# Performance work log

Hardware: AMD Instinct MI355X
Metric: run time of the kernel (lower is better)

The kernel has to match this reference:

```python
import jax, jax.numpy as jnp
import numpy as np

EPS = 1e-5  # torch BatchNorm1d default eps


def _bn(x, gamma, beta):
    # training-mode batch norm over axis 0 (biased variance, like torch)
    m = x.mean(axis=0)
    v = x.var(axis=0)
    return (x - m) * jax.lax.rsqrt(v + EPS) * gamma + beta


def setup_inputs() -> dict:
    key = jax.random.key(0)
    ks = jax.random.split(key, 6)
    B, T, D_IN, E, H, D_OUT = 8192, 64, 2, 128, 128, 5
    s = 0.05
    f32 = jnp.float32
    return {
        "inputs": jax.random.normal(ks[0], (B, T, D_IN), f32),
        # input BatchNorm1d(2)
        "in_gamma": jnp.ones((D_IN,), f32),
        "in_beta": jnp.zeros((D_IN,), f32),
        # input embed MLP: Linear(2->128) + BN(128) + ReLU
        "W_emb": jax.random.normal(ks[1], (E, D_IN), f32) * s,
        "b_emb": jnp.zeros((E,), f32),
        "emb_gamma": jnp.ones((E,), f32),
        "emb_beta": jnp.zeros((E,), f32),
        # LSTMCell(128, 128): gate order i, f, g, o
        "W_ih": jax.random.normal(ks[2], (4 * H, E), f32) * s,
        "W_hh": jax.random.normal(ks[3], (4 * H, H), f32) * s,
        "b_ih": jnp.zeros((4 * H,), f32),
        "b_hh": jnp.zeros((4 * H,), f32),
        # output MLP: Linear(128->5) + BN(5), no activation
        "W_out": jax.random.normal(ks[4], (D_OUT, H), f32) * s,
        "b_out": jnp.zeros((D_OUT,), f32),
        "out_gamma": jnp.ones((D_OUT,), f32),
        "out_beta": jnp.zeros((D_OUT,), f32),
    }


def reference(inputs, in_gamma, in_beta, W_emb, b_emb, emb_gamma, emb_beta,
              W_ih, W_hh, b_ih, b_hh, W_out, b_out, out_gamma, out_beta):
    B, T, D = inputs.shape
    H = W_hh.shape[1]
    # input_norm over flattened (B*T, 2)
    x = _bn(inputs.reshape(-1, D), in_gamma, in_beta).reshape(B, T, D)

    h0 = jnp.zeros((B, H), inputs.dtype)
    c0 = jnp.zeros((B, H), inputs.dtype)

    def step(hc, x_t):
        h, c = hc
        # embed: Linear + BN + ReLU (per-step batch stats, as in torch loop)
        e = jax.nn.relu(_bn(x_t @ W_emb.T + b_emb, emb_gamma, emb_beta))
        gates = e @ W_ih.T + b_ih + h @ W_hh.T + b_hh
        i, f, g, o = jnp.split(gates, 4, axis=-1)
        c_new = jax.nn.sigmoid(f) * c + jax.nn.sigmoid(i) * jnp.tanh(g)
        h_new = jax.nn.sigmoid(o) * jnp.tanh(c_new)
        out = _bn(h_new @ W_out.T + b_out, out_gamma, out_beta)
        return (h_new, c_new), out

    (h, c), outs = jax.lax.scan(step, (h0, c0), jnp.swapaxes(x, 0, 1))
    return jnp.swapaxes(outs, 0, 1), (h, c)  # [B, T, 5], ([B,H],[B,H])
```

## Files before the change

kernel.cpp:

```cpp
#include <hip/hip_runtime.h>
#include <hip/hip_bf16.h>

#define BB 8192
#define TT 64
#define L2E 1.44269504088896f

typedef __attribute__((ext_vector_type(8))) short bf16x8;
typedef __attribute__((ext_vector_type(4))) float f32x4;

__device__ __forceinline__ float exp2g(float x) { return __builtin_amdgcn_exp2f(x); }
__device__ __forceinline__ float rcpg(float x)  { return __builtin_amdgcn_rcpf(x); }
__device__ __forceinline__ short f2bf_s(float x) {
  __hip_bfloat16 b = __float2bfloat16(x);
  return *reinterpret_cast<short*>(&b);
}
__device__ __forceinline__ int aidx(int row, int k) {
  return row * 512 + ((((k >> 3) ^ (row & 7))) << 3) + (k & 7);
}

__global__ void prep_kernel(const float* __restrict__ Wih, const float* __restrict__ Whh,
                            const float* __restrict__ bih, const float* __restrict__ bhh,
                            const float* __restrict__ Wout,
                            short* __restrict__ Wcb, short* __restrict__ Woutb,
                            float* __restrict__ bc) {
  int idx = blockIdx.x * 256 + threadIdx.x;
  if (idx < 16384) {
    int l = idx & 63, f = idx >> 6;
    int kt = f >> 5, nt = f & 31;
    int k0 = kt * 32 + ((l >> 4) << 3);
    int col = nt * 16 + (l & 15);
    int gate = col >> 7;
    float s = (gate == 2) ? (2.f * L2E) : (-L2E);
    const float* src = (k0 < 128) ? (Wih + col * 128 + k0) : (Whh + col * 128 + (k0 - 128));
    bf16x8 v;
    #pragma unroll
    for (int e = 0; e < 8; e++) v[e] = f2bf_s(src[e] * s);
    *(bf16x8*)(Wcb + (size_t)idx * 8) = v;
  } else if (idx < 16640) {
    int i2 = idx - 16384;
    int l = i2 & 63, f = i2 >> 6;
    int k0 = f * 32 + ((l >> 4) << 3);
    int col = l & 15;
    bf16x8 v;
    #pragma unroll
    for (int e = 0; e < 8; e++)
      v[e] = (col < 5) ? f2bf_s(Wout[col * 128 + k0 + e]) : (short)0;
    *(bf16x8*)(Woutb + (size_t)i2 * 8) = v;
  } else {
    int i3 = idx - 16640;
    int gate = i3 >> 7;
    float s = (gate == 2) ? (2.f * L2E) : (-L2E);
    bc[i3] = (bih[i3] + bhh[i3]) * s;
  }
}

__global__ void stats_kernel(const float* __restrict__ x, float* __restrict__ stats) {
  int t = blockIdx.x, tid = threadIdx.x;
  float s0=0, s1=0, s2=0, s3=0, s4=0;
  for (int b = tid; b < BB; b += 256) {
    const float* p = x + ((size_t)b * TT + t) * 2;
    float x0 = p[0], x1 = p[1];
    s0 += x0; s1 += x1; s2 += x0*x0; s3 += x0*x1; s4 += x1*x1;
  }
  __shared__ float red[4][5];
  int lane = tid & 63, w = tid >> 6;
  #pragma unroll
  for (int off = 32; off > 0; off >>= 1) {
    s0 += __shfl_down(s0, off); s1 += __shfl_down(s1, off);
    s2 += __shfl_down(s2, off); s3 += __shfl_down(s3, off); s4 += __shfl_down(s4, off);
  }
  if (lane == 0) { red[w][0]=s0; red[w][1]=s1; red[w][2]=s2; red[w][3]=s3; red[w][4]=s4; }
  __syncthreads();
  if (tid < 5) stats[t*5 + tid] = red[0][tid] + red[1][tid] + red[2][tid] + red[3][tid];
}

__global__ void coef_kernel(const float* __restrict__ stats,
                            const float* __restrict__ Wemb, const float* __restrict__ bemb,
                            const float* __restrict__ ing, const float* __restrict__ inb,
                            const float* __restrict__ eg, const float* __restrict__ eb,
                            float* __restrict__ A0, float* __restrict__ A1, float* __restrict__ Ct) {
  __shared__ float st[64][5];
  __shared__ float glob[4];
  int tid = threadIdx.x;
  for (int i = tid; i < 320; i += 128) st[i / 5][i % 5] = stats[i];
  __syncthreads();
  if (tid == 0) {
    float S0=0, S1=0, S00=0, S11=0;
    for (int t = 0; t < 64; t++) { S0+=st[t][0]; S1+=st[t][1]; S00+=st[t][2]; S11+=st[t][4]; }
    float inv_n = 1.f / (float)(BB * TT);
    float M0 = S0*inv_n, M1 = S1*inv_n;
    float V0 = S00*inv_n - M0*M0, V1 = S11*inv_n - M1*M1;
    float P0 = rsqrtf(V0 + 1e-5f) * ing[0];
    float P1 = rsqrtf(V1 + 1e-5f) * ing[1];
    glob[0]=P0; glob[1]=P1; glob[2]=inb[0]-M0*P0; glob[3]=inb[1]-M1*P1;
  }
  __syncthreads();
  float P0=glob[0], P1=glob[1], Q0=glob[2], Q1=glob[3];
  int j = tid;
  float w0 = Wemb[j*2], w1 = Wemb[j*2+1];
  float a0 = P0*w0, a1 = P1*w1;
  float cj = Q0*w0 + Q1*w1 + bemb[j];
  float gam = eg[j], bet = eb[j];
  float invB = 1.f / (float)BB;
  for (int t = 0; t < 64; t++) {
    float m0 = st[t][0]*invB, m1 = st[t][1]*invB;
    float v00 = st[t][2]*invB - m0*m0;
    float v01 = st[t][3]*invB - m0*m1;
    float v11 = st[t][4]*invB - m1*m1;
    float mean = a0*m0 + a1*m1 + cj;
    float var  = a0*a0*v00 + 2.f*a0*a1*v01 + a1*a1*v11;
    float G = rsqrtf(var + 1e-5f) * gam;
    A0[t*128 + j] = G * a0;
    A1[t*128 + j] = G * a1;
    Ct[t*128 + j] = G * cj + (bet - mean * G);
  }
}

__device__ __forceinline__ void write_e(short* acts_s,
                                        const float* __restrict__ A0, const float* __restrict__ A1,
                                        const float* __restrict__ Ct,
                                        int t, int er, int cg, float x0, float x1) {
  const float4 a0a = *(const float4*)(A0 + t*128 + cg*8);
  const float4 a0b = *(const float4*)(A0 + t*128 + cg*8 + 4);
  const float4 a1a = *(const float4*)(A1 + t*128 + cg*8);
  const float4 a1b = *(const float4*)(A1 + t*128 + cg*8 + 4);
  const float4 cta = *(const float4*)(Ct + t*128 + cg*8);
  const float4 ctb = *(const float4*)(Ct + t*128 + cg*8 + 4);
  bf16x8 v;
  v[0] = f2bf_s(fmaxf(fmaf(a0a.x, x0, fmaf(a1a.x, x1, cta.x)), 0.f));
  v[1] = f2bf_s(fmaxf(fmaf(a0a.y, x0, fmaf(a1a.y, x1, cta.y)), 0.f));
  v[2] = f2bf_s(fmaxf(fmaf(a0a.z, x0, fmaf(a1a.z, x1, cta.z)), 0.f));
  v[3] = f2bf_s(fmaxf(fmaf(a0a.w, x0, fmaf(a1a.w, x1, cta.w)), 0.f));
  v[4] = f2bf_s(fmaxf(fmaf(a0b.x, x0, fmaf(a1b.x, x1, ctb.x)), 0.f));
  v[5] = f2bf_s(fmaxf(fmaf(a0b.y, x0, fmaf(a1b.y, x1, ctb.y)), 0.f));
  v[6] = f2bf_s(fmaxf(fmaf(a0b.z, x0, fmaf(a1b.z, x1, ctb.z)), 0.f));
  v[7] = f2bf_s(fmaxf(fmaf(a0b.w, x0, fmaf(a1b.w, x1, ctb.w)), 0.f));
  int gk = (t & 1) * 16 + cg;
  *(bf16x8*)&acts_s[er * 512 + ((gk ^ (er & 7)) << 3)] = v;
}

__launch_bounds__(512, 1)
__global__ void lstm_kernel(const float* __restrict__ x,
                            const float* __restrict__ A0, const float* __restrict__ A1,
                            const float* __restrict__ Ctab,
                            const short* __restrict__ Wcb, const float* __restrict__ bc,
                            const short* __restrict__ Woutb, const float* __restrict__ bout,
                            float* __restrict__ outy, float* __restrict__ hout,
                            float* __restrict__ cout) {
  __shared__ __align__(16) short acts_s[32 * 512];
  __shared__ __align__(16) float xs[32 * 128];

  const int tid  = threadIdx.x;
  const int lane = tid & 63;
  const int w    = tid >> 6;
  const int row0 = blockIdx.x * 32;
  const int cl   = lane & 15;
  const int lq   = lane >> 4;
  const int er   = tid >> 4;
  const int cg   = tid & 15;

  {
    const float4* src = (const float4*)(x + (size_t)row0 * 128);
    float4* dst = (float4*)xs;
    dst[tid]       = src[tid];
    dst[tid + 512] = src[tid + 512];
  }

  float bgs[4];
  #pragma unroll
  for (int g = 0; g < 4; g++) bgs[g] = bc[g * 128 + w * 16 + cl];
  const float bov = (cl < 5) ? bout[cl] : 0.f;

  bf16x8 wreg[8][4];
  {
    const bf16x8* wptr = (const bf16x8*)Wcb;
    #pragma unroll
    for (int kt = 0; kt < 8; kt++)
      #pragma unroll
      for (int g = 0; g < 4; g++)
        wreg[kt][g] = wptr[(size_t)(kt * 32 + g * 8 + w) * 64 + lane];
  }
  bf16x8 wof[4];
  if ((w & 3) == 0) {
    #pragma unroll
    for (int kyt = 0; kyt < 4; kyt++)
      wof[kyt] = *(const bf16x8*)(Woutb + (size_t)(kyt * 64 + lane) * 8);
  }

  __syncthreads();

  write_e(acts_s, A0, A1, Ctab, 0, er, cg, xs[er * 128], xs[er * 128 + 1]);
  {
    bf16x8 z = (bf16x8)0;
    int gk = 32 + 16 + cg;
    *(bf16x8*)&acts_s[er * 512 + ((gk ^ (er & 7)) << 3)] = z;
  }

  f32x4 cstate[2] = {{0.f,0.f,0.f,0.f},{0.f,0.f,0.f,0.f}};
  float hl[2][4];

  #pragma unroll 1
  for (int t = 0; t < TT; t++) {
    __syncthreads();
    const int ebuf = t & 1;
    const int hbuf = (t + 1) & 1;

    if ((w & 3) == 0 && t > 0) {
      int mty = w >> 2;
      int row = mty * 16 + cl;
      f32x4 ya = (f32x4){0.f,0.f,0.f,0.f};
      #pragma unroll
      for (int kyt = 0; kyt < 4; kyt++) {
        int k = 256 + hbuf * 128 + (kyt * 4 + lq) * 8;
        bf16x8 ah = *(const bf16x8*)&acts_s[aidx(row, k)];
        ya = __builtin_amdgcn_mfma_f32_16x16x32_bf16(ah, wof[kyt], ya, 0, 0, 0);
      }
      if (cl < 5) {
        #pragma unroll
        for (int q = 0; q < 4; q++) {
          int brow = row0 + mty * 16 + lq * 4 + q;
          outy[((size_t)brow * TT + (t - 1)) * 5 + cl] = ya[q] + bov;
        }
      }
    }

    f32x4 acc[4][2];
    #pragma unroll
    for (int g = 0; g < 4; g++)
      #pragma unroll
      for (int mt = 0; mt < 2; mt++)
        acc[g][mt] = (f32x4){bgs[g], bgs[g], bgs[g], bgs[g]};

    #pragma unroll
    for (int kt = 0; kt < 8; kt++) {
      int k = (kt < 4) ? (ebuf * 128 + (kt * 4 + lq) * 8)
                       : (256 + hbuf * 128 + ((kt - 4) * 4 + lq) * 8);
      bf16x8 a0 = *(const bf16x8*)&acts_s[aidx(cl, k)];
      bf16x8 a1 = *(const bf16x8*)&acts_s[aidx(16 + cl, k)];
      #pragma unroll
      for (int g = 0; g < 4; g++) {
        acc[g][0] = __builtin_amdgcn_mfma_f32_16x16x32_bf16(a0, wreg[kt][g], acc[g][0], 0, 0, 0);
        acc[g][1] = __builtin_amdgcn_mfma_f32_16x16x32_bf16(a1, wreg[kt][g], acc[g][1], 0, 0, 0);
      }
    }

    #pragma unroll
    for (int mt = 0; mt < 2; mt++) {
      #pragma unroll
      for (int q = 0; q < 4; q++) {
        float Ei = exp2g(acc[0][mt][q]);
        float Ef = exp2g(acc[1][mt][q]);
        float Eg = exp2g(acc[2][mt][q]);
        float Eo = exp2g(acc[3][mt][q]);
        float di = 1.f + Ei, dg = 1.f + Eg;
        float ig = (Eg - 1.f) * rcpg(di * dg);
        float fv = rcpg(1.f + Ef);
        float cn = fmaf(fv, cstate[mt][q], ig);
        cstate[mt][q] = cn;
        float Ec = exp2g(cn * (2.f * L2E));
        float hn = (Ec - 1.f) * rcpg((1.f + Eo) * (1.f + Ec));
        hl[mt][q] = hn;
        int row = mt * 16 + lq * 4 + q;
        int k   = 256 + (t & 1) * 128 + w * 16 + cl;
        acts_s[aidx(row, k)] = f2bf_s(hn);
      }
    }
    if (t < TT - 1)
      write_e(acts_s, A0, A1, Ctab, t + 1, er, cg,
              xs[er * 128 + (t + 1) * 2], xs[er * 128 + (t + 1) * 2 + 1]);
  }

  __syncthreads();
  if ((w & 3) == 0) {
    int mty = w >> 2;
    int row = mty * 16 + cl;
    int hbuf = TT & 1 ? 0 : 1;
    f32x4 ya = (f32x4){0.f,0.f,0.f,0.f};
    #pragma unroll
    for (int kyt = 0; kyt < 4; kyt++) {
      int k = 256 + ((TT - 1) & 1) * 128 + (kyt * 4 + lq) * 8;
      bf16x8 ah = *(const bf16x8*)&acts_s[aidx(row, k)];
      ya = __builtin_amdgcn_mfma_f32_16x16x32_bf16(ah, wof[kyt], ya, 0, 0, 0);
    }
    (void)hbuf;
    if (cl < 5) {
      #pragma unroll
      for (int q = 0; q < 4; q++) {
        int brow = row0 + mty * 16 + lq * 4 + q;
        outy[((size_t)brow * TT + (TT - 1)) * 5 + cl] = ya[q] + bov;
      }
    }
  }

  #pragma unroll
  for (int mt = 0; mt < 2; mt++) {
    #pragma unroll
    for (int q = 0; q < 4; q++) {
      int brow = row0 + mt * 16 + lq * 4 + q;
      int col  = w * 16 + cl;
      hout[(size_t)brow * 128 + col] = hl[mt][q];
      cout[(size_t)brow * 128 + col] = cstate[mt][q];
    }
  }
}

__global__ void ostats_kernel(const float* __restrict__ outy, float* __restrict__ ost) {
  int t = blockIdx.x, tid = threadIdx.x;
  float s[5] = {0,0,0,0,0}, s2[5] = {0,0,0,0,0};
  for (int b = tid; b < BB; b += 256) {
    const float* p = outy + ((size_t)b * TT + t) * 5;
    #pragma unroll
    for (int k = 0; k < 5; k++) { float v = p[k]; s[k] += v; s2[k] += v*v; }
  }
  __shared__ float red[4][10];
  int lane = tid & 63, w = tid >> 6;
  #pragma unroll
  for (int off = 32; off > 0; off >>= 1) {
    #pragma unroll
    for (int k = 0; k < 5; k++) {
      s[k]  += __shfl_down(s[k], off);
      s2[k] += __shfl_down(s2[k], off);
    }
  }
  if (lane == 0) {
    #pragma unroll
    for (int k = 0; k < 5; k++) { red[w][k] = s[k]; red[w][5+k] = s2[k]; }
  }
  __syncthreads();
  if (tid < 10) ost[t*10 + tid] = red[0][tid]+red[1][tid]+red[2][tid]+red[3][tid];
}

__global__ void onorm_kernel(float* __restrict__ outy, const float* __restrict__ ost,
                             const float* __restrict__ og, const float* __restrict__ ob) {
  const int N = BB*TT*5;
  const float invB = 1.f / (float)BB;
  for (int i = blockIdx.x * 256 + threadIdx.x; i < N; i += gridDim.x * 256) {
    int k = i % 5;
    int t = (i / 5) % TT;
    float m = ost[t*10 + k] * invB;
    float v = ost[t*10 + 5 + k] * invB - m*m;
    outy[i] = (outy[i] - m) * rsqrtf(v + 1e-5f) * og[k] + ob[k];
  }
}

extern "C" void kernel_launch(void* const* d_in, const int* in_sizes, int n_in,
                              void* d_out, int out_size, void* d_ws, size_t ws_size,
                              hipStream_t stream) {
  const float* xin  = (const float*)d_in[0];
  const float* ing  = (const float*)d_in[1];
  const float* inb  = (const float*)d_in[2];
  const float* Wemb = (const float*)d_in[3];
  const float* bemb = (const float*)d_in[4];
  const float* eg   = (const float*)d_in[5];
  const float* eb   = (const float*)d_in[6];
  const float* Wih  = (const float*)d_in[7];
  const float* Whh  = (const float*)d_in[8];
  const float* bih  = (const float*)d_in[9];
  const float* bhh  = (const float*)d_in[10];
  const float* Wout = (const float*)d_in[11];
  const float* bout = (const float*)d_in[12];
  const float* og   = (const float*)d_in[13];
  const float* ob   = (const float*)d_in[14];

  float* ws    = (float*)d_ws;
  float* stats = ws;
  float* A0    = ws + 1024;
  float* A1    = ws + 9216;
  float* Ct    = ws + 17408;
  float* bc    = ws + 25600;
  short* Wcb   = (short*)(ws + 26624);
  short* Woutb = (short*)(ws + 92160);
  float* ost   = ws + 93184;

  float* outy = (float*)d_out;
  float* hout = outy + (size_t)BB * TT * 5;
  float* cout = hout + (size_t)BB * 128;

  prep_kernel <<<67, 256, 0, stream>>>(Wih, Whh, bih, bhh, Wout, Wcb, Woutb, bc);
  stats_kernel<<<64, 256, 0, stream>>>(xin, stats);
  coef_kernel <<<1, 128, 0, stream>>>(stats, Wemb, bemb, ing, inb, eg, eb, A0, A1, Ct);
  lstm_kernel <<<256, 512, 0, stream>>>(xin, A0, A1, Ct, Wcb, bc, Woutb, bout,
                                        outy, hout, cout);
  ostats_kernel<<<64, 256, 0, stream>>>(outy, ost);
  onorm_kernel <<<2048, 256, 0, stream>>>(outy, ost, og, ob);
}
```

Before: 248.4 us.

## Software-pipeline LSTM input projection and split output-stats reduction

Restructures the LSTM step loop so the input-embedding half of the gate GEMM for step t+1 is issued right after the activations of step t. Only the recurrent half then sits on the critical path, and the per-step sync count drops to one. It also writes the embedding two steps ahead and stores final h/c inside the loop. Output weights are reloaded from global memory each step instead of being held in registers, trading register pressure for extra loads. The output-BN stats are split across four times more blocks, with a small finalize kernel that precomputes scale and shift so the normalize pass is a single FMA.

```diff
diff --git a/kernel.cpp b/kernel.cpp
--- a/kernel.cpp
+++ b/kernel.cpp
@@ -16,6 +16,9 @@
 }
 __device__ __forceinline__ int aidx(int row, int k) {
   return row * 512 + ((((k >> 3) ^ (row & 7))) << 3) + (k & 7);
+}
+__device__ __forceinline__ bf16x8 ldg(const short* acts, int row, int kg) {
+  return *(const bf16x8*)&acts[row * 512 + ((kg ^ (row & 7)) << 3)];
 }
 
 __global__ void prep_kernel(const float* __restrict__ Wih, const float* __restrict__ Whh,
@@ -119,13 +122,14 @@
 __device__ __forceinline__ void write_e(short* acts_s,
                                         const float* __restrict__ A0, const float* __restrict__ A1,
                                         const float* __restrict__ Ct,
-                                        int t, int er, int cg, float x0, float x1) {
-  const float4 a0a = *(const float4*)(A0 + t*128 + cg*8);
-  const float4 a0b = *(const float4*)(A0 + t*128 + cg*8 + 4);
-  const float4 a1a = *(const float4*)(A1 + t*128 + cg*8);
-  const float4 a1b = *(const float4*)(A1 + t*128 + cg*8 + 4);
-  const float4 cta = *(const float4*)(Ct + t*128 + cg*8);
-  const float4 ctb = *(const float4*)(Ct + t*128 + cg*8 + 4);
+                                        int t, int er, int cg, const float* __restrict__ xs) {
+  const float* a0p = A0 + t*128 + cg*8;
+  const float* a1p = A1 + t*128 + cg*8;
+  const float* ccp = Ct + t*128 + cg*8;
+  const float4 a0a = *(const float4*)a0p, a0b = *(const float4*)(a0p + 4);
+  const float4 a1a = *(const float4*)a1p, a1b = *(const float4*)(a1p + 4);
+  const float4 cta = *(const float4*)ccp, ctb = *(const float4*)(ccp + 4);
+  float x0 = xs[er * 128 + t * 2], x1 = xs[er * 128 + t * 2 + 1];
   bf16x8 v;
   v[0] = f2bf_s(fmaxf(fmaf(a0a.x, x0, fmaf(a1a.x, x1, cta.x)), 0.f));
   v[1] = f2bf_s(fmaxf(fmaf(a0a.y, x0, fmaf(a1a.y, x1, cta.y)), 0.f));
@@ -180,40 +184,65 @@
       for (int g = 0; g < 4; g++)
         wreg[kt][g] = wptr[(size_t)(kt * 32 + g * 8 + w) * 64 + lane];
   }
-  bf16x8 wof[4];
-  if ((w & 3) == 0) {
-    #pragma unroll
-    for (int kyt = 0; kyt < 4; kyt++)
-      wof[kyt] = *(const bf16x8*)(Woutb + (size_t)(kyt * 64 + lane) * 8);
-  }
-
-  __syncthreads();
-
-  write_e(acts_s, A0, A1, Ctab, 0, er, cg, xs[er * 128], xs[er * 128 + 1]);
+
+  __syncthreads();
+
+  write_e(acts_s, A0, A1, Ctab, 0, er, cg, xs);
   {
     bf16x8 z = (bf16x8)0;
-    int gk = 32 + 16 + cg;
+    int gk = 48 + cg;
     *(bf16x8*)&acts_s[er * 512 + ((gk ^ (er & 7)) << 3)] = z;
   }
+  __syncthreads();
+
+  f32x4 acc[4][2];
+  #pragma unroll
+  for (int g = 0; g < 4; g++) {
+    acc[g][0] = (f32x4){bgs[g], bgs[g], bgs[g], bgs[g]};
+    acc[g][1] = acc[g][0];
+  }
+  #pragma unroll
+  for (int kt = 0; kt < 4; kt++) {
+    bf16x8 a0 = ldg(acts_s, cl, kt * 4 + lq);
+    bf16x8 a1 = ldg(acts_s, 16 + cl, kt * 4 + lq);
+    #pragma unroll
+    for (int g = 0; g < 4; g++) {
+      acc[g][0] = __builtin_amdgcn_mfma_f32_16x16x32_bf16(a0, wreg[kt][g], acc[g][0], 0, 0, 0);
+      acc[g][1] = __builtin_amdgcn_mfma_f32_16x16x32_bf16(a1, wreg[kt][g], acc[g][1], 0, 0, 0);
+    }
+  }
+  write_e(acts_s, A0, A1, Ctab, 1, er, cg, xs);
+  __syncthreads();
 
   f32x4 cstate[2] = {{0.f,0.f,0.f,0.f},{0.f,0.f,0.f,0.f}};
-  float hl[2][4];
 
   #pragma unroll 1
   for (int t = 0; t < TT; t++) {
-    __syncthreads();
-    const int ebuf = t & 1;
-    const int hbuf = (t + 1) & 1;
-
+    const int hb_prev = (t + 1) & 1;
+    const int hb_cur  = t & 1;
+    const int eb_next = (t + 1) & 1;
+
+    #pragma unroll
+    for (int kt = 0; kt < 4; kt++) {
+      int kgh = 32 + hb_prev * 16 + kt * 4 + lq;
+      bf16x8 a0 = ldg(acts_s, cl, kgh);
+      bf16x8 a1 = ldg(acts_s, 16 + cl, kgh);
+      #pragma unroll
+      for (int g = 0; g < 4; g++) {
+        acc[g][0] = __builtin_amdgcn_mfma_f32_16x16x32_bf16(a0, wreg[4 + kt][g], acc[g][0], 0, 0, 0);
+        acc[g][1] = __builtin_amdgcn_mfma_f32_16x16x32_bf16(a1, wreg[4 + kt][g], acc[g][1], 0, 0, 0);
+      }
+    }
+
+    if (t < TT - 2) write_e(acts_s, A0, A1, Ctab, t + 2, er, cg, xs);
     if ((w & 3) == 0 && t > 0) {
       int mty = w >> 2;
-      int row = mty * 16 + cl;
-      f32x4 ya = (f32x4){0.f,0.f,0.f,0.f};
+      f32x4 ya = (f32x4){0.f, 0.f, 0.f, 0.f};
       #pragma unroll
       for (int kyt = 0; kyt < 4; kyt++) {
-        int k = 256 + hbuf * 128 + (kyt * 4 + lq) * 8;
-        bf16x8 ah = *(const bf16x8*)&acts_s[aidx(row, k)];
-        ya = __builtin_amdgcn_mfma_f32_16x16x32_bf16(ah, wof[kyt], ya, 0, 0, 0);
+        bf16x8 wo = *(const bf16x8*)(Woutb + (size_t)(kyt * 64 + lane) * 8);
+        bf16x8 ah = ldg(acts_s, mty * 16 + cl, 32 + hb_prev * 16 + kyt * 4 + lq);
+        ya = __builtin_amdgcn_mfma_f32_16x16x32_bf16(ah, wo, ya, 0, 0, 0);
       }
       if (cl < 5) {
         #pragma unroll
@@ -221,26 +250,6 @@
           int brow = row0 + mty * 16 + lq * 4 + q;
           outy[((size_t)brow * TT + (t - 1)) * 5 + cl] = ya[q] + bov;
         }
-      }
-    }
-
-    f32x4 acc[4][2];
-    #pragma unroll
-    for (int g = 0; g < 4; g++)
-      #pragma unroll
-      for (int mt = 0; mt < 2; mt++)
-        acc[g][mt] = (f32x4){bgs[g], bgs[g], bgs[g], bgs[g]};
-
-    #pragma unroll
-    for (int kt = 0; kt < 8; kt++) {
-      int k = (kt < 4) ? (ebuf * 128 + (kt * 4 + lq) * 8)
-                       : (256 + hbuf * 128 + ((kt - 4) * 4 + lq) * 8);
-      bf16x8 a0 = *(const bf16x8*)&acts_s[aidx(cl, k)];
-      bf16x8 a1 = *(const bf16x8*)&acts_s[aidx(16 + cl, k)];
-      #pragma unroll
-      for (int g = 0; g < 4; g++) {
-        acc[g][0] = __builtin_amdgcn_mfma_f32_16x16x32_bf16(a0, wreg[kt][g], acc[g][0], 0, 0, 0);
-        acc[g][1] = __builtin_amdgcn_mfma_f32_16x16x32_bf16(a1, wreg[kt][g], acc[g][1], 0, 0, 0);
       }
     }
 
@@ -252,37 +261,46 @@
         float Ef = exp2g(acc[1][mt][q]);
         float Eg = exp2g(acc[2][mt][q]);
         float Eo = exp2g(acc[3][mt][q]);
-        float di = 1.f + Ei, dg = 1.f + Eg;
-        float ig = (Eg - 1.f) * rcpg(di * dg);
+        float ig = (Eg - 1.f) * rcpg((1.f + Ei) * (1.f + Eg));
         float fv = rcpg(1.f + Ef);
         float cn = fmaf(fv, cstate[mt][q], ig);
         cstate[mt][q] = cn;
         float Ec = exp2g(cn * (2.f * L2E));
         float hn = (Ec - 1.f) * rcpg((1.f + Eo) * (1.f + Ec));
-        hl[mt][q] = hn;
         int row = mt * 16 + lq * 4 + q;
-        int k   = 256 + (t & 1) * 128 + w * 16 + cl;
+        int k   = 256 + hb_cur * 128 + w * 16 + cl;
         acts_s[aidx(row, k)] = f2bf_s(hn);
-      }
-    }
-    if (t < TT - 1)
-      write_e(acts_s, A0, A1, Ctab, t + 1, er, cg,
-              xs[er * 128 + (t + 1) * 2], xs[er * 128 + (t + 1) * 2 + 1]);
-  }
-
-  __syncthreads();
+        if (t == TT - 1) {
+          hout[(size_t)(row0 + row) * 128 + w * 16 + cl] = hn;
+          cout[(size_t)(row0 + row) * 128 + w * 16 + cl] = cn;
+        }
+      }
+      if (t < TT - 1) {
+        #pragma unroll
+        for (int g = 0; g < 4; g++)
+          acc[g][mt] = (f32x4){bgs[g], bgs[g], bgs[g], bgs[g]};
+        #pragma unroll
+        for (int kt = 0; kt < 4; kt++) {
+          bf16x8 a = ldg(acts_s, mt * 16 + cl, eb_next * 16 + kt * 4 + lq);
+          #pragma unroll
+          for (int g = 0; g < 4; g++)
+            acc[g][mt] = __builtin_amdgcn_mfma_f32_16x16x32_bf16(a, wreg[kt][g], acc[g][mt], 0, 0, 0);
+        }
+      }
+    }
+
+    __syncthreads();
+  }
+
   if ((w & 3) == 0) {
     int mty = w >> 2;
-    int row = mty * 16 + cl;
-    int hbuf = TT & 1 ? 0 : 1;
-    f32x4 ya = (f32x4){0.f,0.f,0.f,0.f};
+    f32x4 ya = (f32x4){0.f, 0.f, 0.f, 0.f};
     #pragma unroll
     for (int kyt = 0; kyt < 4; kyt++) {
-      int k = 256 + ((TT - 1) & 1) * 128 + (kyt * 4 + lq) * 8;
-      bf16x8 ah = *(const bf16x8*)&acts_s[aidx(row, k)];
-      ya = __builtin_amdgcn_mfma_f32_16x16x32_bf16(ah, wof[kyt], ya, 0, 0, 0);
-    }
-    (void)hbuf;
+      bf16x8 wo = *(const bf16x8*)(Woutb + (size_t)(kyt * 64 + lane) * 8);
+      bf16x8 ah = ldg(acts_s, mty * 16 + cl, 32 + ((TT - 1) & 1) * 16 + kyt * 4 + lq);
+      ya = __builtin_amdgcn_mfma_f32_16x16x32_bf16(ah, wo, ya, 0, 0, 0);
+    }
     if (cl < 5) {
       #pragma unroll
       for (int q = 0; q < 4; q++) {
@@ -291,23 +309,14 @@
       }
     }
   }
-
-  #pragma unroll
-  for (int mt = 0; mt < 2; mt++) {
-    #pragma unroll
-    for (int q = 0; q < 4; q++) {
-      int brow = row0 + mt * 16 + lq * 4 + q;
-      int col  = w * 16 + cl;
-      hout[(size_t)brow * 128 + col] = hl[mt][q];
-      cout[(size_t)brow * 128 + col] = cstate[mt][q];
-    }
-  }
-}
-
-__global__ void ostats_kernel(const float* __restrict__ outy, float* __restrict__ ost) {
-  int t = blockIdx.x, tid = threadIdx.x;
+}
+
+__global__ void ostats_kernel(const float* __restrict__ outy, float* __restrict__ ostp) {
+  int t = blockIdx.x >> 2, part = blockIdx.x & 3;
+  int tid = threadIdx.x;
   float s[5] = {0,0,0,0,0}, s2[5] = {0,0,0,0,0};
-  for (int b = tid; b < BB; b += 256) {
+  int b0 = part * 2048;
+  for (int b = b0 + tid; b < b0 + 2048; b += 256) {
     const float* p = outy + ((size_t)b * TT + t) * 5;
     #pragma unroll
     for (int k = 0; k < 5; k++) { float v = p[k]; s[k] += v; s2[k] += v*v; }
@@ -327,19 +336,30 @@
     for (int k = 0; k < 5; k++) { red[w][k] = s[k]; red[w][5+k] = s2[k]; }
   }
   __syncthreads();
-  if (tid < 10) ost[t*10 + tid] = red[0][tid]+red[1][tid]+red[2][tid]+red[3][tid];
-}
-
-__global__ void onorm_kernel(float* __restrict__ outy, const float* __restrict__ ost,
-                             const float* __restrict__ og, const float* __restrict__ ob) {
-  const int N = BB*TT*5;
+  if (tid < 10) ostp[blockIdx.x * 10 + tid] = red[0][tid]+red[1][tid]+red[2][tid]+red[3][tid];
+}
+
+__global__ void ofin_kernel(const float* __restrict__ ostp,
+                            const float* __restrict__ og, const float* __restrict__ ob,
+                            float* __restrict__ sc, float* __restrict__ sh) {
+  int i = threadIdx.x;
+  if (i >= 320) return;
+  int t = i / 5, k = i - t * 5;
   const float invB = 1.f / (float)BB;
+  float m  = (ostp[(t*4+0)*10+k]   + ostp[(t*4+1)*10+k]   + ostp[(t*4+2)*10+k]   + ostp[(t*4+3)*10+k]) * invB;
+  float s2 = (ostp[(t*4+0)*10+5+k] + ostp[(t*4+1)*10+5+k] + ostp[(t*4+2)*10+5+k] + ostp[(t*4+3)*10+5+k]) * invB;
+  float v = s2 - m * m;
+  float scale = rsqrtf(v + 1e-5f) * og[k];
+  sc[i] = scale;
+  sh[i] = ob[k] - m * scale;
+}
+
+__global__ void onorm_kernel(float* __restrict__ outy, const float* __restrict__ sc,
+                             const float* __restrict__ sh) {
+  const int N = BB * TT * 5;
   for (int i = blockIdx.x * 256 + threadIdx.x; i < N; i += gridDim.x * 256) {
-    int k = i % 5;
-    int t = (i / 5) % TT;
-    float m = ost[t*10 + k] * invB;
-    float v = ost[t*10 + 5 + k] * invB - m*m;
-    outy[i] = (outy[i] - m) * rsqrtf(v + 1e-5f) * og[k] + ob[k];
+    int j = i % 320;
+    outy[i] = fmaf(outy[i], sc[j], sh[j]);
   }
 }
 
@@ -370,7 +390,9 @@
   float* bc    = ws + 25600;
   short* Wcb   = (short*)(ws + 26624);
   short* Woutb = (short*)(ws + 92160);
-  float* ost   = ws + 93184;
+  float* ostp  = ws + 93184;
+  float* sc    = ws + 95744;
+  float* sh    = ws + 96064;
 
   float* outy = (float*)d_out;
   float* hout = outy + (size_t)BB * TT * 5;
@@ -381,6 +403,7 @@
   coef_kernel <<<1, 128, 0, stream>>>(stats, Wemb, bemb, ing, inb, eg, eb, A0, A1, Ct);
   lstm_kernel <<<256, 512, 0, stream>>>(xin, A0, A1, Ct, Wcb, bc, Woutb, bout,
                                         outy, hout, cout);
-  ostats_kernel<<<64, 256, 0, stream>>>(outy, ost);
-  onorm_kernel <<<2048, 256, 0, stream>>>(outy, ost, og, ob);
-}
+  ostats_kernel<<<256, 256, 0, stream>>>(outy, ostp);
+  ofin_kernel <<<1, 320, 0, stream>>>(ostp, og, ob, sc, sh);
+  onorm_kernel<<<2048, 256, 0, stream>>>(outy, sc, sh);
+}
```

After: 305.2 us (median of 2 runs). 1.23x slower.
